# Kernel optimization log

Hardware: AMD Instinct MI355X
Metric: run time of the kernel (lower is better)

## Reference

```python
import jax, jax.numpy as jnp
import numpy as np

B, C, H, W = 4, 256, 32, 32
NUM_HEADS = 8
DK = C // NUM_HEADS


def _conv1x1(x_bcn, Wt, b):
    # x_bcn: [B, C, N]; Wt: [C_out, C_in]; b: [C_out]
    return jnp.einsum('oc,bcn->bon', Wt, x_bcn) + b[None, :, None]


def setup_inputs() -> dict:
    key = jax.random.key(0)
    ks = jax.random.split(key, 12)
    shp = (B, C, H, W)
    s = 1.0 / np.sqrt(C)
    return {
        'x0': jax.random.normal(ks[0], shp, jnp.float32),
        'x1': jax.random.normal(ks[1], shp, jnp.float32),
        'x2': jax.random.normal(ks[2], shp, jnp.float32),
        'gamma': jnp.ones((1,), jnp.float32),
        'gamma_1': jnp.ones((1,), jnp.float32),
        'gamma_2': jnp.ones((1,), jnp.float32),
        'Wq': jax.random.normal(ks[3], (C, C), jnp.float32) * s,
        'bq': jnp.zeros((C,), jnp.float32),
        'Wk': jax.random.normal(ks[4], (C, C), jnp.float32) * s,
        'bk': jnp.zeros((C,), jnp.float32),
        'Wv': jax.random.normal(ks[5], (C, C), jnp.float32) * s,
        'bv': jnp.zeros((C,), jnp.float32),
        'Wo': jax.random.normal(ks[6], (C, C), jnp.float32) * s,
        'bo': jnp.zeros((C,), jnp.float32),
    }


def reference(x0, x1, x2, gamma, gamma_1, gamma_2, Wq, bq, Wk, bk, Wv, bv, Wo, bo):
    h, dk = NUM_HEADS, DK
    N = H * W
    s0 = gamma * x0
    s1 = gamma_1 * x1
    s2 = gamma_2 * x2
    s0f = s0.reshape(B, C, N)
    streams = jnp.stack([s0f, s1.reshape(B, C, N), s2.reshape(B, C, N)], axis=1)  # [B,3,C,N]
    # Q: [B, h, N, dk]
    Q = _conv1x1(s0f, Wq, bq).reshape(B, h, dk, N).transpose(0, 1, 3, 2)
    kv_in = streams.reshape(B * 3, C, N)
    # K, V: [B, 3, h, dk, N] -> [B, h, 3N, dk]
    K = _conv1x1(kv_in, Wk, bk).reshape(B, 3, h, dk, N).transpose(0, 2, 1, 4, 3).reshape(B, h, 3 * N, dk)
    V = _conv1x1(kv_in, Wv, bv).reshape(B, 3, h, dk, N).transpose(0, 2, 1, 4, 3).reshape(B, h, 3 * N, dk)
    scores = jnp.einsum('bhqd,bhkd->bhqk', Q, K) / jnp.sqrt(jnp.float32(dk))  # [B,h,N,3N]
    attn = jax.nn.softmax(scores, axis=-1)
    out = jnp.einsum('bhqk,bhkd->bhqd', attn, V)  # [B,h,N,dk]
    out = out.transpose(0, 1, 3, 2).reshape(B, C, N)  # [B,C,N]
    fused = _conv1x1(out, Wo, bo).reshape(B, C, H, W)
    return fused
```

## Files before the change

### kernel.cpp

```cpp
#include <hip/hip_runtime.h>

typedef short bf16x8 __attribute__((ext_vector_type(8)));
typedef float f32x4  __attribute__((ext_vector_type(4)));
typedef short sh4    __attribute__((ext_vector_type(4)));
typedef float fl4    __attribute__((ext_vector_type(4)));
typedef unsigned u32x2 __attribute__((ext_vector_type(2)));
typedef unsigned u32x4 __attribute__((ext_vector_type(4)));

#define B_N  4
#define C_N  256
#define NH_N 8
#define DK_N 32
#define N_N  1024
#define KN_N 3072

#if defined(__has_builtin)
#if __has_builtin(__builtin_amdgcn_permlane32_swap) && __has_builtin(__builtin_amdgcn_permlane16_swap)
#define USE_PERMLANE 1
#endif
#endif
#ifndef USE_PERMLANE
#define USE_PERMLANE 0
#endif

__device__ __forceinline__ short f2bf(float f) {
    union { float f; unsigned u; } v; v.f = f;
    unsigned r = v.u + 0x7fffu + ((v.u >> 16) & 1u);
    return (short)(r >> 16);
}
__device__ __forceinline__ unsigned fbits(float f) {
    union { float f; unsigned u; } v; v.f = f; return v.u;
}

__global__ __launch_bounds__(256) void prep_kernel(
    const float* __restrict__ x0, const float* __restrict__ x1,
    const float* __restrict__ x2, const float* __restrict__ g0,
    const float* __restrict__ g1, const float* __restrict__ g2,
    const float* __restrict__ Wq, const float* __restrict__ Wk,
    const float* __restrict__ Wv, const float* __restrict__ Wo,
    short* __restrict__ Xt, short* __restrict__ Wbf) {
    if (blockIdx.z == 12) {
        int t = (blockIdx.y * 16 + blockIdx.x) * 256 + threadIdx.x;
#pragma unroll
        for (int m = 0; m < 4; ++m) {
            const float* src = (m == 0) ? Wq : (m == 1) ? Wk : (m == 2) ? Wv : Wo;
            fl4 v = *reinterpret_cast<const fl4*>(src + t * 4);
            sh4 o;
            o.x = f2bf(v.x); o.y = f2bf(v.y); o.z = f2bf(v.z); o.w = f2bf(v.w);
            *reinterpret_cast<sh4*>(Wbf + m * 65536 + t * 4) = o;
        }
        return;
    }
    __shared__ float tile[64][65];
    int bs = blockIdx.z; int b = bs / 3; int s = bs - b * 3;
    int c0 = blockIdx.y * 64, n0 = blockIdx.x * 64;
    const float* xs = (s == 0) ? x0 : (s == 1) ? x1 : x2;
    float g = (s == 0) ? g0[0] : (s == 1) ? g1[0] : g2[0];
    int tx = threadIdx.x & 63, ty = threadIdx.x >> 6;
    const float* src = xs + (b * C_N + c0) * N_N + n0;
#pragma unroll
    for (int r = 0; r < 16; ++r) {
        int cl = ty * 16 + r;
        tile[cl][tx] = src[cl * N_N + tx] * g;
    }
    __syncthreads();
    short* dst = Xt + ((size_t)bs * N_N + n0) * C_N + c0;
#pragma unroll
    for (int r = 0; r < 16; ++r) {
        int nl = ty * 16 + r;
        dst[nl * C_N + tx] = f2bf(tile[tx][nl]);
    }
}

__global__ __launch_bounds__(256) void qkv_kernel(
    const short* __restrict__ Wbf, const float* __restrict__ bq,
    const float* __restrict__ bk, const float* __restrict__ bv,
    const short* __restrict__ Xt, short* __restrict__ Qs,
    short* __restrict__ Ks, short* __restrict__ Vt) {
    __shared__ short SM[5120];
    int b = blockIdx.z, mt = blockIdx.y, ct = blockIdx.x;
    int lane = threadIdx.x & 63, w = threadIdx.x >> 6;
    int l16 = lane & 15, quad = lane >> 4;
    int m0 = mt * 64;

    int type, s, n0;
    if (ct < 16)      { type = 0; s = 0;                 n0 = ct * 64; }
    else if (ct < 64) { type = 1; int c2 = ct - 16; s = c2 >> 4; n0 = (c2 & 15) * 64; }
    else              { type = 2; int c2 = ct - 64; s = c2 >> 4; n0 = (c2 & 15) * 64; }

    f32x4 acc[4];
#pragma unroll
    for (int i = 0; i < 4; ++i) acc[i] = f32x4{0.f, 0.f, 0.f, 0.f};

    if (type < 2) {
        const short* A    = Wbf + type * 65536;
        const float* bias = (type == 0) ? bq : bk;
        const short* Bsrc = Xt + ((size_t)(b * 3 + s) * N_N + n0) * C_N;
        int arow = m0 + w * 16 + l16;
#pragma unroll
        for (int kc = 0; kc < 256; kc += 32) {
            bf16x8 a = *reinterpret_cast<const bf16x8*>(A + arow * C_N + kc + quad * 8);
#pragma unroll
            for (int nt = 0; nt < 4; ++nt) {
                bf16x8 bb = *reinterpret_cast<const bf16x8*>(Bsrc + (nt * 16 + l16) * C_N + kc + quad * 8);
                acc[nt] = __builtin_amdgcn_mfma_f32_16x16x32_bf16(a, bb, acc[nt], 0, 0, 0);
            }
        }
        const float QSCALE = 0.17677669529663687f * 1.4426950408889634f;
        int row0 = m0 + w * 16 + quad * 4;
        float b0_ = bias[row0], b1_ = bias[row0 + 1], b2_ = bias[row0 + 2], b3_ = bias[row0 + 3];
        int dk0 = (w & 1) * 16 + quad * 4;
        short* Tp = SM + (w >> 1) * 2560 + dk0;
#pragma unroll
        for (int nt = 0; nt < 4; ++nt) {
            int pos = nt * 16 + l16;
            float v0 = acc[nt][0] + b0_, v1 = acc[nt][1] + b1_;
            float v2 = acc[nt][2] + b2_, v3 = acc[nt][3] + b3_;
            sh4 pk;
            if (type == 0) {
                pk.x = f2bf(v0 * QSCALE); pk.y = f2bf(v1 * QSCALE);
                pk.z = f2bf(v2 * QSCALE); pk.w = f2bf(v3 * QSCALE);
            } else {
                pk.x = f2bf(v0); pk.y = f2bf(v1); pk.z = f2bf(v2); pk.w = f2bf(v3);
            }
            *reinterpret_cast<sh4*>(Tp + pos * 40) = pk;
        }
        __syncthreads();
        int t = threadIdx.x;
        int pos_l = t >> 2, seg = t & 3;
#pragma unroll
        for (int hl = 0; hl < 2; ++hl) {
            bf16x8 vv = *reinterpret_cast<const bf16x8*>(SM + hl * 2560 + pos_l * 40 + seg * 8);
            int h = 2 * mt + hl;
            if (type == 0) {
                size_t base = ((size_t)(b * NH_N + h) * N_N + n0) * DK_N;
                *reinterpret_cast<bf16x8*>(Qs + base + t * 8) = vv;
            } else {
                size_t base = ((size_t)(b * NH_N + h) * KN_N + s * N_N + n0) * DK_N;
                *reinterpret_cast<bf16x8*>(Ks + base + t * 8) = vv;
            }
        }
    } else {
        const short* Bw   = Wbf + 2 * 65536;
        const short* Asrc = Xt + (size_t)(b * 3 + s) * N_N * C_N;
        int apos = n0 + w * 16 + l16;
#pragma unroll
        for (int kc = 0; kc < 256; kc += 32) {
            bf16x8 ax = *reinterpret_cast<const bf16x8*>(Asrc + (size_t)apos * C_N + kc + quad * 8);
#pragma unroll
            for (int c2 = 0; c2 < 4; ++c2) {
                bf16x8 bw = *reinterpret_cast<const bf16x8*>(Bw + (size_t)(m0 + c2 * 16 + l16) * C_N + kc + quad * 8);
                acc[c2] = __builtin_amdgcn_mfma_f32_16x16x32_bf16(ax, bw, acc[c2], 0, 0, 0);
            }
        }
        int key0 = w * 16 + quad * 4;
#pragma unroll
        for (int c2 = 0; c2 < 4; ++c2) {
            int row = c2 * 16 + l16;
            float bb_ = bv[m0 + row];
            sh4 pk;
            pk.x = f2bf(acc[c2][0] + bb_); pk.y = f2bf(acc[c2][1] + bb_);
            pk.z = f2bf(acc[c2][2] + bb_); pk.w = f2bf(acc[c2][3] + bb_);
            *reinterpret_cast<sh4*>(SM + row * 72 + key0) = pk;
        }
        __syncthreads();
        int t = threadIdx.x;
#pragma unroll
        for (int i = 0; i < 2; ++i) {
            int ch = t + i * 256;
            int row = ch >> 3, seg = ch & 7;
            bf16x8 vv = *reinterpret_cast<const bf16x8*>(SM + row * 72 + seg * 8);
            int co = m0 + row;
            int h = co >> 5, d = co & 31;
            *reinterpret_cast<bf16x8*>(
                Vt + ((size_t)(b * NH_N + h) * DK_N + d) * KN_N + s * N_N + n0 + seg * 8) = vv;
        }
    }
}

struct Frags { bf16x8 k0, k1, k2, k3, v00, v01, v10, v11; };

__device__ __forceinline__ Frags ldfr(const short* Kp, const short* Vp0, int k0) {
    Frags f;
    f.k0  = *reinterpret_cast<const bf16x8*>(Kp + (k0 +  0) * DK_N);
    f.k1  = *reinterpret_cast<const bf16x8*>(Kp + (k0 + 16) * DK_N);
    f.k2  = *reinterpret_cast<const bf16x8*>(Kp + (k0 + 32) * DK_N);
    f.k3  = *reinterpret_cast<const bf16x8*>(Kp + (k0 + 48) * DK_N);
    f.v00 = *reinterpret_cast<const bf16x8*>(Vp0 + k0);
    f.v01 = *reinterpret_cast<const bf16x8*>(Vp0 + 16 * KN_N + k0);
    f.v10 = *reinterpret_cast<const bf16x8*>(Vp0 + k0 + 32);
    f.v11 = *reinterpret_cast<const bf16x8*>(Vp0 + 16 * KN_N + k0 + 32);
    return f;
}

#define EXPPACK(sv, Ra, Rb, LACC) {                             \
    float p0 = __builtin_amdgcn_exp2f(sv[0]);                   \
    float p1 = __builtin_amdgcn_exp2f(sv[1]);                   \
    float p2 = __builtin_amdgcn_exp2f(sv[2]);                   \
    float p3 = __builtin_amdgcn_exp2f(sv[3]);                   \
    LACC += (p0 + p1) + (p2 + p3);                              \
    Ra = __builtin_amdgcn_perm(fbits(p1), fbits(p0), 0x07060302u); \
    Rb = __builtin_amdgcn_perm(fbits(p3), fbits(p2), 0x07060302u); \
}

#if USE_PERMLANE
#define PVSTEP(RA0, RA1, RB0, RB1, VF0, VF1, O0, O1) {                 \
    unsigned x0 = RA0, y0 = RB0, x1 = RA1, y1 = RB1;                   \
    u32x2 r_;                                                          \
    r_ = __builtin_amdgcn_permlane32_swap(x0, y0, false, false); x0 = r_.x; y0 = r_.y; \
    r_ = __builtin_amdgcn_permlane16_swap(x0, y0, false, false); x0 = r_.x; y0 = r_.y; \
    r_ = __builtin_amdgcn_permlane32_swap(x1, y1, false, false); x1 = r_.x; y1 = r_.y; \
    r_ = __builtin_amdgcn_permlane16_swap(x1, y1, false, false); x1 = r_.x; y1 = r_.y; \
    union { u32x4 u; bf16x8 b; } pf_; pf_.u = u32x4{x0, x1, y0, y1};   \
    O0 = __builtin_amdgcn_mfma_f32_16x16x32_bf16(VF0, pf_.b, O0, 0, 0, 0); \
    O1 = __builtin_amdgcn_mfma_f32_16x16x32_bf16(VF1, pf_.b, O1, 0, 0, 0); \
}
#else
#define PVSTEP(RA0, RA1, RB0, RB1, VF0, VF1, O0, O1) {                 \
    union { u32x2 u; sh4 s; } wa_, wb_;                                \
    wa_.u = u32x2{RA0, RA1}; wb_.u = u32x2{RB0, RB1};                  \
    *reinterpret_cast<sh4*>(&PT[w][l16][quad * 4])      = wa_.s;       \
    *reinterpret_cast<sh4*>(&PT[w][l16][16 + quad * 4]) = wb_.s;       \
    bf16x8 pf_ = *reinterpret_cast<bf16x8*>(&PT[w][l16][quad * 8]);    \
    O0 = __builtin_amdgcn_mfma_f32_16x16x32_bf16(VF0, pf_, O0, 0, 0, 0); \
    O1 = __builtin_amdgcn_mfma_f32_16x16x32_bf16(VF1, pf_, O1, 0, 0, 0); \
}
#endif

#define PROCJ(f, QF, LACC, O0, O1) {                                     \
    f32x4 s0 = __builtin_amdgcn_mfma_f32_16x16x32_bf16(f.k0, QF, zero, 0, 0, 0); \
    f32x4 s1 = __builtin_amdgcn_mfma_f32_16x16x32_bf16(f.k1, QF, zero, 0, 0, 0); \
    f32x4 s2 = __builtin_amdgcn_mfma_f32_16x16x32_bf16(f.k2, QF, zero, 0, 0, 0); \
    f32x4 s3 = __builtin_amdgcn_mfma_f32_16x16x32_bf16(f.k3, QF, zero, 0, 0, 0); \
    unsigned R00, R01, R10, R11, R20, R21, R30, R31;                     \
    EXPPACK(s0, R00, R01, LACC); EXPPACK(s1, R10, R11, LACC);            \
    EXPPACK(s2, R20, R21, LACC); EXPPACK(s3, R30, R31, LACC);            \
    PVSTEP(R00, R01, R10, R11, f.v00, f.v01, O0, O1);                    \
    PVSTEP(R20, R21, R30, R31, f.v10, f.v11, O0, O1);                    \
}

#define PROCALL(f) {                                                     \
    PROCJ(f, qf0, la0, o00, o01);                                        \
    PROCJ(f, qf1, la1, o10, o11);                                        \
    PROCJ(f, qf2, la2, o20, o21);                                        \
    PROCJ(f, qf3, la3, o30, o31);                                        \
}

__global__ __launch_bounds__(256, 2) void attn_kernel(
    const short* __restrict__ Qs, const short* __restrict__ Ks,
    const short* __restrict__ Vt, short* __restrict__ Ot) {
    __shared__ float OL[4][64][36];
    __shared__ float Ll[4][64];
#if !USE_PERMLANE
    __shared__ short PT[4][16][36];
#endif

    int bh = blockIdx.x;
    int q0 = blockIdx.y * 64;
    int t = threadIdx.x, lane = t & 63, w = t >> 6;
    int l16 = lane & 15, quad = lane >> 4;

    const short* Qbase = Qs + ((size_t)bh * N_N + q0 + l16) * DK_N + quad * 8;
    bf16x8 qf0 = *reinterpret_cast<const bf16x8*>(Qbase + 0 * 16 * DK_N);
    bf16x8 qf1 = *reinterpret_cast<const bf16x8*>(Qbase + 1 * 16 * DK_N);
    bf16x8 qf2 = *reinterpret_cast<const bf16x8*>(Qbase + 2 * 16 * DK_N);
    bf16x8 qf3 = *reinterpret_cast<const bf16x8*>(Qbase + 3 * 16 * DK_N);
    const short* Kp  = Ks + ((size_t)bh * KN_N + l16) * DK_N + quad * 8;
    const short* Vp0 = Vt + ((size_t)bh * DK_N + l16) * KN_N + quad * 8;

    const f32x4 zero = {0.f, 0.f, 0.f, 0.f};
    f32x4 o00 = zero, o01 = zero, o10 = zero, o11 = zero;
    f32x4 o20 = zero, o21 = zero, o30 = zero, o31 = zero;
    float la0 = 0.f, la1 = 0.f, la2 = 0.f, la3 = 0.f;
    int kbase = w * 768;

    Frags cur = ldfr(Kp, Vp0, kbase);
#pragma unroll 2
    for (int i = 0; i < 11; ++i) {
        Frags nxt = ldfr(Kp, Vp0, kbase + (i + 1) * 64);
        PROCALL(cur);
        cur = nxt;
    }
    PROCALL(cur);

    la0 += __shfl_xor(la0, 16); la0 += __shfl_xor(la0, 32);
    la1 += __shfl_xor(la1, 16); la1 += __shfl_xor(la1, 32);
    la2 += __shfl_xor(la2, 16); la2 += __shfl_xor(la2, 32);
    la3 += __shfl_xor(la3, 16); la3 += __shfl_xor(la3, 32);

    *reinterpret_cast<fl4*>(&OL[w][ 0 + l16][quad * 4])      = o00;
    *reinterpret_cast<fl4*>(&OL[w][ 0 + l16][16 + quad * 4]) = o01;
    *reinterpret_cast<fl4*>(&OL[w][16 + l16][quad * 4])      = o10;
    *reinterpret_cast<fl4*>(&OL[w][16 + l16][16 + quad * 4]) = o11;
    *reinterpret_cast<fl4*>(&OL[w][32 + l16][quad * 4])      = o20;
    *reinterpret_cast<fl4*>(&OL[w][32 + l16][16 + quad * 4]) = o21;
    *reinterpret_cast<fl4*>(&OL[w][48 + l16][quad * 4])      = o30;
    *reinterpret_cast<fl4*>(&OL[w][48 + l16][16 + quad * 4]) = o31;
    if (quad == 0) {
        Ll[w][ 0 + l16] = la0;
        Ll[w][16 + l16] = la1;
        Ll[w][32 + l16] = la2;
        Ll[w][48 + l16] = la3;
    }
    __syncthreads();

    int q = t >> 2, d0 = (t & 3) * 8;
    float rl = 1.0f / (Ll[0][q] + Ll[1][q] + Ll[2][q] + Ll[3][q]);
    fl4 a0 = *reinterpret_cast<fl4*>(&OL[0][q][d0]);
    fl4 a1 = *reinterpret_cast<fl4*>(&OL[0][q][d0 + 4]);
#pragma unroll
    for (int s = 1; s < 4; ++s) {
        fl4 b0 = *reinterpret_cast<fl4*>(&OL[s][q][d0]);
        fl4 b1 = *reinterpret_cast<fl4*>(&OL[s][q][d0 + 4]);
        a0.x += b0.x; a0.y += b0.y; a0.z += b0.z; a0.w += b0.w;
        a1.x += b1.x; a1.y += b1.y; a1.z += b1.z; a1.w += b1.w;
    }
    union { sh4 s[2]; bf16x8 v; } pk;
    pk.s[0].x = f2bf(a0.x * rl); pk.s[0].y = f2bf(a0.y * rl);
    pk.s[0].z = f2bf(a0.z * rl); pk.s[0].w = f2bf(a0.w * rl);
    pk.s[1].x = f2bf(a1.x * rl); pk.s[1].y = f2bf(a1.y * rl);
    pk.s[1].z = f2bf(a1.z * rl); pk.s[1].w = f2bf(a1.w * rl);
    int b = bh >> 3, h = bh & 7;
    *reinterpret_cast<bf16x8*>(
        Ot + ((size_t)b * N_N + q0 + q) * C_N + h * DK_N + d0) = pk.v;
}

__global__ __launch_bounds__(256) void oproj_kernel(
    const short* __restrict__ Wo_bf, const float* __restrict__ bo,
    const short* __restrict__ Ot, float* __restrict__ out) {
    int b = blockIdx.z, mt = blockIdx.y, ct = blockIdx.x;
    int lane = threadIdx.x & 63, w = threadIdx.x >> 6;
    int l16 = lane & 15, quad = lane >> 4;
    int m0 = mt * 64, n0 = ct * 32;
    const short* Bsrc = Ot + ((size_t)b * N_N + n0) * C_N;
    int arow = m0 + w * 16 + l16;

    f32x4 acc[2];
    acc[0] = f32x4{0.f, 0.f, 0.f, 0.f};
    acc[1] = f32x4{0.f, 0.f, 0.f, 0.f};

#pragma unroll
    for (int kc = 0; kc < 256; kc += 32) {
        bf16x8 a = *reinterpret_cast<const bf16x8*>(Wo_bf + arow * C_N + kc + quad * 8);
#pragma unroll
        for (int nt = 0; nt < 2; ++nt) {
            bf16x8 bb = *reinterpret_cast<const bf16x8*>(Bsrc + (nt * 16 + l16) * C_N + kc + quad * 8);
            acc[nt] = __builtin_amdgcn_mfma_f32_16x16x32_bf16(a, bb, acc[nt], 0, 0, 0);
        }
    }

#pragma unroll
    for (int r = 0; r < 4; ++r) {
        int row = m0 + w * 16 + quad * 4 + r;
        float bias = bo[row];
#pragma unroll
        for (int nt = 0; nt < 2; ++nt) {
            out[((size_t)b * C_N + row) * N_N + n0 + nt * 16 + l16] = acc[nt][r] + bias;
        }
    }
}

extern "C" void kernel_launch(void* const* d_in, const int* in_sizes, int n_in,
                              void* d_out, int out_size, void* d_ws, size_t ws_size,
                              hipStream_t stream) {
    const float* x0 = (const float*)d_in[0];
    const float* x1 = (const float*)d_in[1];
    const float* x2 = (const float*)d_in[2];
    const float* g0 = (const float*)d_in[3];
    const float* g1 = (const float*)d_in[4];
    const float* g2 = (const float*)d_in[5];
    const float* Wq = (const float*)d_in[6];
    const float* bq = (const float*)d_in[7];
    const float* Wk = (const float*)d_in[8];
    const float* bk = (const float*)d_in[9];
    const float* Wv = (const float*)d_in[10];
    const float* bv = (const float*)d_in[11];
    const float* Wo = (const float*)d_in[12];
    const float* bo = (const float*)d_in[13];
    float* out = (float*)d_out;

    char* wsb = (char*)d_ws;
    short* Wbf = (short*)(wsb + 0);
    short* Xt  = (short*)(wsb + 524288);
    short* Qs  = (short*)(wsb + 6815744);
    short* Ks  = (short*)(wsb + 8912896);
    short* Vt  = (short*)(wsb + 15204352);
    short* Ot  = (short*)(wsb + 21495808);

    prep_kernel<<<dim3(16, 4, 13), 256, 0, stream>>>(x0, x1, x2, g0, g1, g2,
                                                     Wq, Wk, Wv, Wo, Xt, Wbf);
    qkv_kernel<<<dim3(112, 4, 4), 256, 0, stream>>>(Wbf, bq, bk, bv, Xt, Qs, Ks, Vt);
    attn_kernel<<<dim3(32, 16), 256, 0, stream>>>(Qs, Ks, Vt, Ot);
    oproj_kernel<<<dim3(32, 4, 4), 256, 0, stream>>>(Wbf + 3 * 65536, bo, Ot, out);
}
```

Measured before the change: 156.5 us.

## Fuse input scaling/transpose/bf16 conversion into QKV projection kernel

```diff
diff --git a/kernel.cpp b/kernel.cpp
--- a/kernel.cpp
+++ b/kernel.cpp
@@ -32,52 +32,33 @@
     union { float f; unsigned u; } v; v.f = f; return v.u;
 }
 
-__global__ __launch_bounds__(256) void prep_kernel(
+__global__ __launch_bounds__(256) void wcvt_kernel(
+    const float* __restrict__ Wq, const float* __restrict__ Wk,
+    const float* __restrict__ Wv, const float* __restrict__ Wo,
+    short* __restrict__ dst) {
+    int t = blockIdx.x * 256 + threadIdx.x;
+    int e = t * 4;
+    int m = e >> 16;
+    int off = e & 65535;
+    const float* src = (m == 0) ? Wq : (m == 1) ? Wk : (m == 2) ? Wv : Wo;
+    fl4 v = *reinterpret_cast<const fl4*>(src + off);
+    sh4 o;
+    o.x = f2bf(v.x); o.y = f2bf(v.y); o.z = f2bf(v.z); o.w = f2bf(v.w);
+    *reinterpret_cast<sh4*>(dst + m * 65536 + off) = o;
+}
+
+__global__ __launch_bounds__(256) void qkv_kernel(
+    const short* __restrict__ Wbf, const float* __restrict__ bq,
+    const float* __restrict__ bk, const float* __restrict__ bv,
     const float* __restrict__ x0, const float* __restrict__ x1,
     const float* __restrict__ x2, const float* __restrict__ g0,
     const float* __restrict__ g1, const float* __restrict__ g2,
-    const float* __restrict__ Wq, const float* __restrict__ Wk,
-    const float* __restrict__ Wv, const float* __restrict__ Wo,
-    short* __restrict__ Xt, short* __restrict__ Wbf) {
-    if (blockIdx.z == 12) {
-        int t = (blockIdx.y * 16 + blockIdx.x) * 256 + threadIdx.x;
-#pragma unroll
-        for (int m = 0; m < 4; ++m) {
-            const float* src = (m == 0) ? Wq : (m == 1) ? Wk : (m == 2) ? Wv : Wo;
-            fl4 v = *reinterpret_cast<const fl4*>(src + t * 4);
-            sh4 o;
-            o.x = f2bf(v.x); o.y = f2bf(v.y); o.z = f2bf(v.z); o.w = f2bf(v.w);
-            *reinterpret_cast<sh4*>(Wbf + m * 65536 + t * 4) = o;
-        }
-        return;
-    }
-    __shared__ float tile[64][65];
-    int bs = blockIdx.z; int b = bs / 3; int s = bs - b * 3;
-    int c0 = blockIdx.y * 64, n0 = blockIdx.x * 64;
-    const float* xs = (s == 0) ? x0 : (s == 1) ? x1 : x2;
-    float g = (s == 0) ? g0[0] : (s == 1) ? g1[0] : g2[0];
-    int tx = threadIdx.x & 63, ty = threadIdx.x >> 6;
-    const float* src = xs + (b * C_N + c0) * N_N + n0;
-#pragma unroll
-    for (int r = 0; r < 16; ++r) {
-        int cl = ty * 16 + r;
-        tile[cl][tx] = src[cl * N_N + tx] * g;
-    }
-    __syncthreads();
-    short* dst = Xt + ((size_t)bs * N_N + n0) * C_N + c0;
-#pragma unroll
-    for (int r = 0; r < 16; ++r) {
-        int nl = ty * 16 + r;
-        dst[nl * C_N + tx] = f2bf(tile[tx][nl]);
-    }
-}
-
-__global__ __launch_bounds__(256) void qkv_kernel(
-    const short* __restrict__ Wbf, const float* __restrict__ bq,
-    const float* __restrict__ bk, const float* __restrict__ bv,
-    const short* __restrict__ Xt, short* __restrict__ Qs,
-    short* __restrict__ Ks, short* __restrict__ Vt) {
-    __shared__ short SM[5120];
+    short* __restrict__ Qs, short* __restrict__ Ks, short* __restrict__ Vt) {
+    __shared__ char smem[16640];
+    __shared__ short Bt[64][264];
+    float (*stage)[65] = reinterpret_cast<float(*)[65]>(smem);
+    short* SM = reinterpret_cast<short*>(smem);
+
     int b = blockIdx.z, mt = blockIdx.y, ct = blockIdx.x;
     int lane = threadIdx.x & 63, w = threadIdx.x >> 6;
     int l16 = lane & 15, quad = lane >> 4;
@@ -88,6 +69,27 @@
     else if (ct < 64) { type = 1; int c2 = ct - 16; s = c2 >> 4; n0 = (c2 & 15) * 64; }
     else              { type = 2; int c2 = ct - 64; s = c2 >> 4; n0 = (c2 & 15) * 64; }
 
+    const float* xs = (s == 0) ? x0 : (s == 1) ? x1 : x2;
+    float g = (s == 0) ? g0[0] : (s == 1) ? g1[0] : g2[0];
+    int tx = threadIdx.x & 63, ty = threadIdx.x >> 6;
+#pragma unroll
+    for (int cb = 0; cb < 4; ++cb) {
+        int c0 = cb * 64;
+        const float* src = xs + ((size_t)(b * C_N + c0)) * N_N + n0;
+#pragma unroll
+        for (int r = 0; r < 16; ++r) {
+            int cl = ty * 16 + r;
+            stage[cl][tx] = src[cl * N_N + tx] * g;
+        }
+        __syncthreads();
+#pragma unroll
+        for (int r = 0; r < 16; ++r) {
+            int nl = ty * 16 + r;
+            Bt[nl][c0 + tx] = f2bf(stage[tx][nl]);
+        }
+        __syncthreads();
+    }
+
     f32x4 acc[4];
 #pragma unroll
     for (int i = 0; i < 4; ++i) acc[i] = f32x4{0.f, 0.f, 0.f, 0.f};
@@ -95,14 +97,13 @@
     if (type < 2) {
         const short* A    = Wbf + type * 65536;
         const float* bias = (type == 0) ? bq : bk;
-        const short* Bsrc = Xt + ((size_t)(b * 3 + s) * N_N + n0) * C_N;
         int arow = m0 + w * 16 + l16;
 #pragma unroll
         for (int kc = 0; kc < 256; kc += 32) {
             bf16x8 a = *reinterpret_cast<const bf16x8*>(A + arow * C_N + kc + quad * 8);
 #pragma unroll
             for (int nt = 0; nt < 4; ++nt) {
-                bf16x8 bb = *reinterpret_cast<const bf16x8*>(Bsrc + (nt * 16 + l16) * C_N + kc + quad * 8);
+                bf16x8 bb = *reinterpret_cast<const bf16x8*>(&Bt[nt * 16 + l16][kc + quad * 8]);
                 acc[nt] = __builtin_amdgcn_mfma_f32_16x16x32_bf16(a, bb, acc[nt], 0, 0, 0);
             }
         }
@@ -141,12 +142,10 @@
             }
         }
     } else {
-        const short* Bw   = Wbf + 2 * 65536;
-        const short* Asrc = Xt + (size_t)(b * 3 + s) * N_N * C_N;
-        int apos = n0 + w * 16 + l16;
+        const short* Bw = Wbf + 2 * 65536;
 #pragma unroll
         for (int kc = 0; kc < 256; kc += 32) {
-            bf16x8 ax = *reinterpret_cast<const bf16x8*>(Asrc + (size_t)apos * C_N + kc + quad * 8);
+            bf16x8 ax = *reinterpret_cast<const bf16x8*>(&Bt[w * 16 + l16][kc + quad * 8]);
 #pragma unroll
             for (int c2 = 0; c2 < 4; ++c2) {
                 bf16x8 bw = *reinterpret_cast<const bf16x8*>(Bw + (size_t)(m0 + c2 * 16 + l16) * C_N + kc + quad * 8);
@@ -381,15 +380,15 @@
 
     char* wsb = (char*)d_ws;
     short* Wbf = (short*)(wsb + 0);
-    short* Xt  = (short*)(wsb + 524288);
     short* Qs  = (short*)(wsb + 6815744);
     short* Ks  = (short*)(wsb + 8912896);
     short* Vt  = (short*)(wsb + 15204352);
     short* Ot  = (short*)(wsb + 21495808);
 
-    prep_kernel<<<dim3(16, 4, 13), 256, 0, stream>>>(x0, x1, x2, g0, g1, g2,
-                                                     Wq, Wk, Wv, Wo, Xt, Wbf);
-    qkv_kernel<<<dim3(112, 4, 4), 256, 0, stream>>>(Wbf, bq, bk, bv, Xt, Qs, Ks, Vt);
+    wcvt_kernel<<<256, 256, 0, stream>>>(Wq, Wk, Wv, Wo, Wbf);
+    qkv_kernel<<<dim3(112, 4, 4), 256, 0, stream>>>(Wbf, bq, bk, bv,
+                                                    x0, x1, x2, g0, g1, g2,
+                                                    Qs, Ks, Vt);
     attn_kernel<<<dim3(32, 16), 256, 0, stream>>>(Qs, Ks, Vt, Ot);
     oproj_kernel<<<dim3(32, 4, 4), 256, 0, stream>>>(Wbf + 3 * 65536, bo, Ot, out);
 }
```

New measurement: 149.1 us. -4.8%, faster.
